# Kernel tuning notes

Measured on AMD Instinct MI355X. Metric: run time of the kernel, lower is better.

The kernel has to match this reference:

```python
import jax, jax.numpy as jnp
import numpy as np

SCALE = 8      # scale_factor from map_to_mat_info
PATCH = 32     # up_delta - low_delta + 1 == right_delta - left_delta + 1 (uniform interior patches)


def setup_inputs() -> dict:
    key = jax.random.key(0)
    mat_h, mat_w = 160, 160
    H = (mat_h - 1) * SCALE + PATCH  # 1304: deltas (0,31,0,31) -> no border clipping
    W = (mat_w - 1) * SCALE + PATCH
    x = jax.random.normal(key, (1, 3, H, W), dtype=jnp.float32)
    rgb_weight = jnp.array([0.299, 0.587, 0.114], dtype=jnp.float32).reshape(1, 3, 1, 1)
    return {"x": x, "rgb_weight": rgb_weight, "mat_h": mat_h, "mat_w": mat_w}


def reference(x, rgb_weight, mat_h, mat_w):
    P = PATCH
    # RGB -> grayscale (convert_gray branch for in_channels == 3)
    gray = jnp.sum(x * rgb_weight, axis=1)[0]  # (H, W)
    # Gather all overlapping PxP patches at stride SCALE -> (mat_h, mat_w, P, P)
    rows = (jnp.arange(mat_h) * SCALE)[:, None] + jnp.arange(P)[None, :]  # (mat_h, P)
    cols = (jnp.arange(mat_w) * SCALE)[:, None] + jnp.arange(P)[None, :]  # (mat_w, P)
    p = gray[rows.reshape(-1)].reshape(mat_h, P, -1)              # (mat_h, P, W)
    p = p[:, :, cols.reshape(-1)].reshape(mat_h, P, mat_w, P)     # (mat_h, P, mat_w, P)
    patches = jnp.transpose(p, (0, 2, 1, 3))                      # (mat_h, mat_w, P, P)
    # torch.rfft(signal_ndim=2, onesided=False) == full 2D FFT; power = re^2 + im^2
    F = jnp.fft.fft2(patches)
    log_power = jnp.log(F.real * F.real + F.imag * F.imag + 1.0)
    # High-frequency region sums (h == w == P, static)
    lo = P // 2 - P // 4 - 1   # 7
    up = P // 2 + P // 4       # 24
    r1 = jnp.sum(log_power[..., lo:up + 1, :], axis=(-2, -1))
    r2 = jnp.sum(log_power[..., up + 1:, lo:up + 1], axis=(-2, -1))
    r3 = jnp.sum(log_power[..., :lo, lo:up + 1], axis=(-2, -1))
    mat = (r1 + r2 + r3)[None, None]  # (1, 1, mat_h, mat_w)
    return mat / jnp.max(mat)
```

## Files before the change

### kernel.cpp

```cpp
#include <hip/hip_runtime.h>
#include <math.h>

#define SCALE 8
#define PSZ 32

__device__ constexpr float C32[16] = {
     1.000000000000000f,  0.980785280403230f,  0.923879532511287f,  0.831469612302545f,
     0.707106781186548f,  0.555570233019602f,  0.382683432365090f,  0.195090322016128f,
     0.000000000000000f, -0.195090322016128f, -0.382683432365090f, -0.555570233019602f,
    -0.707106781186548f, -0.831469612302545f, -0.923879532511287f, -0.980785280403230f };
__device__ constexpr float S32[16] = {
     0.000000000000000f,  0.195090322016128f,  0.382683432365090f,  0.555570233019602f,
     0.707106781186548f,  0.831469612302545f,  0.923879532511287f,  0.980785280403230f,
     1.000000000000000f,  0.980785280403230f,  0.923879532511287f,  0.831469612302545f,
     0.707106781186548f,  0.555570233019602f,  0.382683432365090f,  0.195090322016128f };

__device__ __forceinline__ constexpr int brev4(int i) {
    return ((i & 1) << 3) | ((i & 2) << 1) | ((i & 4) >> 1) | ((i & 8) >> 3);
}

__device__ __forceinline__ void fft16(float re[16], float im[16]) {
#pragma unroll
    for (int i = 0; i < 16; ++i) {
        const int j = brev4(i);
        if (j > i) {
            float t = re[i]; re[i] = re[j]; re[j] = t;
            t = im[i]; im[i] = im[j]; im[j] = t;
        }
    }
#pragma unroll
    for (int s = 1; s <= 4; ++s) {
        const int m = 1 << s;
        const int h = m >> 1;
        const int tstep = 32 >> s;
#pragma unroll
        for (int k = 0; k < 16; k += m) {
#pragma unroll
            for (int j = 0; j < h; ++j) {
                const float wr = C32[j * tstep];
                const float wi = -S32[j * tstep];
                const int a = k + j;
                const int b = k + j + h;
                const float tr = wr * re[b] - wi * im[b];
                const float ti = wr * im[b] + wi * re[b];
                re[b] = re[a] - tr; im[b] = im[a] - ti;
                re[a] = re[a] + tr; im[a] = im[a] + ti;
            }
        }
    }
}

__device__ __forceinline__ unsigned pack_bf2(float hi, float lo) {
    const unsigned uh = __float_as_uint(hi) + 0x8000u;
    const unsigned ul = __float_as_uint(lo) + 0x8000u;
    return (uh & 0xFFFF0000u) | (ul >> 16);
}
__device__ __forceinline__ float bf_hi(unsigned u) { return __uint_as_float(u & 0xFFFF0000u); }
__device__ __forceinline__ float bf_lo(unsigned u) { return __uint_as_float(u << 16); }

__global__ __launch_bounds__(256) void gray_kernel(
        const float* __restrict__ x, const float* __restrict__ w,
        float* __restrict__ g, int n4, long long HW) {
    const int i = blockIdx.x * 256 + threadIdx.x;
    if (i >= n4) return;
    const float w0 = w[0], w1 = w[1], w2 = w[2];
    const float4 a = reinterpret_cast<const float4*>(x)[i];
    const float4 b = reinterpret_cast<const float4*>(x + HW)[i];
    const float4 c = reinterpret_cast<const float4*>(x + 2 * HW)[i];
    float4 o;
    o.x = w0 * a.x + w1 * b.x + w2 * c.x;
    o.y = w0 * a.y + w1 * b.y + w2 * c.y;
    o.z = w0 * a.z + w1 * b.z + w2 * c.z;
    o.w = w0 * a.w + w1 * b.w + w2 * c.w;
    reinterpret_cast<float4*>(g)[i] = o;
}

template <bool GRAY_PRE>
__global__ __launch_bounds__(128) void hfdft_patch_kernel(
        const float* __restrict__ x, const float* __restrict__ w,
        float* __restrict__ out, int H, int W, int mat_h, int mat_w) {
    __shared__ unsigned cb[8 * 528];

    const int tid = threadIdx.x;
    const int wid = tid >> 6;
    const int lane = tid & 63;
    const int P0 = blockIdx.x * 8 + wid * 4;
    const int total = mat_h * mat_w;
    const long long HW = (long long)H * W;
    unsigned* cbw = cb + wid * 4 * 528;

    {
        const int g = lane >> 5, r = lane & 31;
        int pA = P0 + 2 * g;
        if (pA > total - 1) pA = total - 1;
        int pB = pA + 1; if (pB > total - 1) pB = total - 1;
        const int phA = pA / mat_w, pwA = pA % mat_w;
        const int phB = pB / mat_w, pwB = pB % mat_w;
        const bool adj = (phA == phB) && (pwB == pwA + 1);
        const int baseA = (phA * SCALE + r) * W + pwA * SCALE;
        const int baseB = (phB * SCALE + r) * W + pwB * SCALE;
        const float w0 = GRAY_PRE ? 0.0f : w[0];
        const float w1 = GRAY_PRE ? 0.0f : w[1];
        const float w2 = GRAY_PRE ? 0.0f : w[2];

        unsigned* cbA = cbw + (2 * g) * 528;
        unsigned* cbB = cbA + 528;


        {
            float win[40];
            if (GRAY_PRE && adj) {
                const float4* g4 = reinterpret_cast<const float4*>(x + baseA);
#pragma unroll
                for (int q = 0; q < 10; ++q) {
                    const float4 v = g4[q];
                    win[4 * q + 0] = v.x; win[4 * q + 1] = v.y;
                    win[4 * q + 2] = v.z; win[4 * q + 3] = v.w;
                }
            } else if (GRAY_PRE) {
#pragma unroll
                for (int i = 0; i < 32; ++i) win[i] = x[baseA + i];
#pragma unroll
                for (int i = 0; i < 8; ++i) win[32 + i] = 0.0f;
            } else {
#pragma unroll
                for (int i = 0; i < 32; ++i)
                    win[i] = w0 * x[baseA + i] + w1 * x[HW + baseA + i] + w2 * x[2 * HW + baseA + i];
#pragma unroll
                for (int i = 0; i < 8; ++i) win[32 + i] = 0.0f;
            }
            float er[16], ei[16];
            if (GRAY_PRE && adj) {
#pragma unroll
                for (int i = 0; i < 16; ++i) {
                    er[i] = win[i] + win[i + 16];
                    ei[i] = win[i + 8] + win[i + 24];
                }
            } else if (GRAY_PRE) {
#pragma unroll
                for (int i = 0; i < 16; ++i) {
                    er[i] = win[i] + win[i + 16];
                    ei[i] = x[baseB + i] + x[baseB + i + 16];
                }
            } else {
#pragma unroll
                for (int i = 0; i < 16; ++i) {
                    er[i] = win[i] + win[i + 16];
                    const float blo = w0 * x[baseB + i] + w1 * x[HW + baseB + i] + w2 * x[2 * HW + baseB + i];
                    const float bhi = w0 * x[baseB + i + 16] + w1 * x[HW + baseB + i + 16] + w2 * x[2 * HW + baseB + i + 16];
                    ei[i] = blo + bhi;
                }
            }
            fft16(er, ei);
            cbA[r] = pack_bf2(er[0], er[8]);
            cbB[r] = pack_bf2(ei[0], ei[8]);
#pragma unroll
            for (int k2 = 1; k2 <= 7; ++k2) {
                const int e1 = k2, e2 = 16 - k2;
                const float far_ = 0.5f * (er[e1] + er[e2]);
                const float fai_ = 0.5f * (ei[e1] - ei[e2]);
                const float fbr_ = 0.5f * (ei[e1] + ei[e2]);
                const float fbi_ = 0.5f * (er[e2] - er[e1]);
                cbA[(2 * k2) * 33 + r] = pack_bf2(far_, fai_);
                cbB[(2 * k2) * 33 + r] = pack_bf2(fbr_, fbi_);
            }
        }

        asm volatile("" ::: "memory");

        {
            float win[40];
            if (GRAY_PRE && adj) {
                const float4* g4 = reinterpret_cast<const float4*>(x + baseA);
#pragma unroll
                for (int q = 0; q < 10; ++q) {
                    const float4 v = g4[q];
                    win[4 * q + 0] = v.x; win[4 * q + 1] = v.y;
                    win[4 * q + 2] = v.z; win[4 * q + 3] = v.w;
                }
            } else if (GRAY_PRE) {
#pragma unroll
                for (int i = 0; i < 32; ++i) win[i] = x[baseA + i];
#pragma unroll
                for (int i = 0; i < 8; ++i) win[32 + i] = 0.0f;
            } else {
#pragma unroll
                for (int i = 0; i < 32; ++i)
                    win[i] = w0 * x[baseA + i] + w1 * x[HW + baseA + i] + w2 * x[2 * HW + baseA + i];
#pragma unroll
                for (int i = 0; i < 8; ++i) win[32 + i] = 0.0f;
            }
            float orr[16], oi[16];
#pragma unroll
            for (int i = 0; i < 16; ++i) {
                float dre, dim;
                if (GRAY_PRE && adj) {
                    dre = win[i] - win[i + 16];
                    dim = win[i + 8] - win[i + 24];
                } else if (GRAY_PRE) {
                    dre = win[i] - win[i + 16];
                    dim = x[baseB + i] - x[baseB + i + 16];
                } else {
                    dre = win[i] - win[i + 16];
                    const float blo = w0 * x[baseB + i] + w1 * x[HW + baseB + i] + w2 * x[2 * HW + baseB + i];
                    const float bhi = w0 * x[baseB + i + 16] + w1 * x[HW + baseB + i + 16] + w2 * x[2 * HW + baseB + i + 16];
                    dim = blo - bhi;
                }
                orr[i] = dre * C32[i] + dim * S32[i];
                oi[i]  = dim * C32[i] - dre * S32[i];
            }
            fft16(orr, oi);
#pragma unroll
            for (int k2 = 0; k2 <= 7; ++k2) {
                const int o1 = k2, o2 = 15 - k2;
                const float far_ = 0.5f * (orr[o1] + orr[o2]);
                const float fai_ = 0.5f * (oi[o1] - oi[o2]);
                const float fbr_ = 0.5f * (oi[o1] + oi[o2]);
                const float fbi_ = 0.5f * (orr[o2] - orr[o1]);
                cbA[(2 * k2 + 1) * 33 + r] = pack_bf2(far_, fai_);
                cbB[(2 * k2 + 1) * 33 + r] = pack_bf2(fbr_, fbi_);
            }
        }
    }

    asm volatile("s_waitcnt lgkmcnt(0)" ::: "memory");

    {
        const int pl = lane >> 4, slot = lane & 15;
        const int p = P0 + pl;
        const unsigned* cbp = cbw + pl * 528 + slot * 33;
        const float b1f = (slot >= 7) ? 1.0f : 0.0f;
        const float m1f = (slot >= 8) ? 1.0f : 0.0f;

        float s0 = 0.0f, s1 = 0.0f;

        {
            float er[16], ei[16];
#pragma unroll
            for (int i = 0; i < 16; ++i) {
                const unsigned u0 = cbp[i], u1 = cbp[i + 16];
                er[i] = bf_hi(u0) + bf_hi(u1);
                ei[i] = bf_lo(u0) + bf_lo(u1);
            }
            fft16(er, ei);
            if (slot == 0) {
#pragma unroll
                for (int k2 = 0; k2 <= 8; ++k2) {
                    const int kr = 2 * k2;
                    const int a = k2, b = (k2 == 0) ? 0 : 16 - k2;
                    const float g0r = 0.5f * (er[a] + er[b]);
                    const float g0i = 0.5f * (ei[a] - ei[b]);
                    const float g1r = 0.5f * (ei[a] + ei[b]);
                    const float g1i = 0.5f * (er[b] - er[a]);
                    const float w0c = (kr >= 7 ? 1.0f : 0.0f) + ((kr >= 8 && kr <= 15) ? 1.0f : 0.0f);
                    const float w16c = 1.0f + ((kr >= 1 && kr <= 15) ? 1.0f : 0.0f);
                    if (w0c > 0.0f)
                        s0 = fmaf(w0c, __logf(g0r * g0r + g0i * g0i + 1.0f), s0);
                    s1 = fmaf(w16c, __logf(g1r * g1r + g1i * g1i + 1.0f), s1);
                }
            } else {
#pragma unroll
                for (int k2 = 0; k2 < 16; ++k2) {
                    const int kr = 2 * k2;
                    const float lp = __logf(er[k2] * er[k2] + ei[k2] * ei[k2] + 1.0f);
                    const float wgt = (kr >= 8 && kr <= 24) ? 2.0f : (b1f + m1f);
                    if (k2 & 1) s1 = fmaf(wgt, lp, s1);
                    else        s0 = fmaf(wgt, lp, s0);
                }
            }
        }

        asm volatile("" ::: "memory");

        {
            float orr[16], oi[16];
#pragma unroll
            for (int i = 0; i < 16; ++i) {
                const unsigned u0 = cbp[i], u1 = cbp[i + 16];
                const float dre = bf_hi(u0) - bf_hi(u1);
                const float dim = bf_lo(u0) - bf_lo(u1);
                orr[i] = dre * C32[i] + dim * S32[i];
                oi[i]  = dim * C32[i] - dre * S32[i];
            }
            fft16(orr, oi);
            if (slot == 0) {
#pragma unroll
                for (int k2 = 0; k2 <= 7; ++k2) {
                    const int kr = 2 * k2 + 1;
                    const int a = k2, b = 15 - k2;
                    const float g0r = 0.5f * (orr[a] + orr[b]);
                    const float g0i = 0.5f * (oi[a] - oi[b]);
                    const float g1r = 0.5f * (oi[a] + oi[b]);
                    const float g1i = 0.5f * (orr[b] - orr[a]);
                    const float w0c = (kr >= 7 ? 1.0f : 0.0f) + ((kr >= 8 && kr <= 15) ? 1.0f : 0.0f);
                    const float w16c = 2.0f;
                    if (w0c > 0.0f)
                        s0 = fmaf(w0c, __logf(g0r * g0r + g0i * g0i + 1.0f), s0);
                    s1 = fmaf(w16c, __logf(g1r * g1r + g1i * g1i + 1.0f), s1);
                }
            } else {
#pragma unroll
                for (int k2 = 0; k2 < 16; ++k2) {
                    const int kr = 2 * k2 + 1;
                    const float lp = __logf(orr[k2] * orr[k2] + oi[k2] * oi[k2] + 1.0f);
                    float wgt;
                    if (kr == 7)                   wgt = 1.0f + m1f;
                    else if (kr == 25)             wgt = b1f + 1.0f;
                    else if (kr >= 9 && kr <= 23)  wgt = 2.0f;
                    else                           wgt = b1f + m1f;
                    if (k2 & 1) s1 = fmaf(wgt, lp, s1);
                    else        s0 = fmaf(wgt, lp, s0);
                }
            }
        }

        float s = s0 + s1;
#pragma unroll
        for (int off = 8; off >= 1; off >>= 1) s += __shfl_xor(s, off, 16);
        if (slot == 0 && p < total) out[p] = s;
    }
}

__global__ __launch_bounds__(1024) void max_kernel(
        const float* __restrict__ sums, int n, float* __restrict__ partial) {
    __shared__ float sm[16];
    float m = 0.0f;
    for (int i = blockIdx.x * 1024 + threadIdx.x; i < n; i += gridDim.x * 1024)
        m = fmaxf(m, sums[i]);
#pragma unroll
    for (int off = 32; off >= 1; off >>= 1) m = fmaxf(m, __shfl_xor(m, off, 64));
    if ((threadIdx.x & 63) == 0) sm[threadIdx.x >> 6] = m;
    __syncthreads();
    if (threadIdx.x == 0) {
#pragma unroll
        for (int i = 1; i < 16; ++i) m = fmaxf(m, sm[i]);
        partial[blockIdx.x] = m;
    }
}

__global__ __launch_bounds__(256) void norm_kernel(
        float* __restrict__ out, int n, const float* __restrict__ partial) {
    const int i = blockIdx.x * 256 + threadIdx.x;
    float m = partial[0];
#pragma unroll
    for (int b = 1; b < 8; ++b) m = fmaxf(m, partial[b]);
    if (i < n) out[i] = out[i] / m;
}

extern "C" void kernel_launch(void* const* d_in, const int* in_sizes, int n_in,
                              void* d_out, int out_size, void* d_ws, size_t ws_size,
                              hipStream_t stream) {
    const float* x = (const float*)d_in[0];
    const float* w = (const float*)d_in[1];
    float* out = (float*)d_out;

    const int HWi = in_sizes[0] / 3;
    const int H = (int)(sqrt((double)HWi) + 0.5);
    const int W = H;
    const long long HW = (long long)H * W;
    const int mat = (int)(sqrt((double)out_size) + 0.5);
    const int total = mat * mat;
    const int blocksA = (total + 7) / 8;

    float* partial = (float*)d_ws;
    float* gray = (float*)((char*)d_ws + 256);
    const size_t need = 256 + (size_t)HW * 4;

    if (ws_size >= need && (W & 3) == 0) {
        const int n4 = (int)(HW / 4);
        hipLaunchKernelGGL(gray_kernel, dim3((n4 + 255) / 256), dim3(256), 0, stream,
                           x, w, gray, n4, HW);
        hipLaunchKernelGGL((hfdft_patch_kernel<true>), dim3(blocksA), dim3(128), 0, stream,
                           gray, w, out, H, W, mat, mat);
    } else {
        hipLaunchKernelGGL((hfdft_patch_kernel<false>), dim3(blocksA), dim3(128), 0, stream,
                           x, w, out, H, W, mat, mat);
    }
    hipLaunchKernelGGL(max_kernel, dim3(8), dim3(1024), 0, stream, out, total, partial);
    hipLaunchKernelGGL(norm_kernel, dim3((total + 255) / 256), dim3(256), 0, stream,
                       out, total, partial);
}
```

Measured before the change: 46.02 us.

## Split even/odd FFT halves across two wavefronts per patch group

```diff
diff --git a/kernel.cpp b/kernel.cpp
--- a/kernel.cpp
+++ b/kernel.cpp
@@ -79,19 +79,19 @@
 __global__ __launch_bounds__(128) void hfdft_patch_kernel(
         const float* __restrict__ x, const float* __restrict__ w,
         float* __restrict__ out, int H, int W, int mat_h, int mat_w) {
-    __shared__ unsigned cb[8 * 528];
+    __shared__ unsigned cb[4 * 528];
+    __shared__ float red[8];
 
     const int tid = threadIdx.x;
-    const int wid = tid >> 6;
+    const int h = tid >> 6;
     const int lane = tid & 63;
-    const int P0 = blockIdx.x * 8 + wid * 4;
     const int total = mat_h * mat_w;
     const long long HW = (long long)H * W;
-    unsigned* cbw = cb + wid * 4 * 528;
+    const int Pbase = blockIdx.x * 4;
 
     {
         const int g = lane >> 5, r = lane & 31;
-        int pA = P0 + 2 * g;
+        int pA = Pbase + 2 * g;
         if (pA > total - 1) pA = total - 1;
         int pB = pA + 1; if (pB > total - 1) pB = total - 1;
         const int phA = pA / mat_w, pwA = pA % mat_w;
@@ -99,159 +99,119 @@
         const bool adj = (phA == phB) && (pwB == pwA + 1);
         const int baseA = (phA * SCALE + r) * W + pwA * SCALE;
         const int baseB = (phB * SCALE + r) * W + pwB * SCALE;
-        const float w0 = GRAY_PRE ? 0.0f : w[0];
-        const float w1 = GRAY_PRE ? 0.0f : w[1];
-        const float w2 = GRAY_PRE ? 0.0f : w[2];
-
-        unsigned* cbA = cbw + (2 * g) * 528;
+
+        float ar[32], br[32];
+        if (GRAY_PRE && adj) {
+            float win[40];
+            const float4* g4 = reinterpret_cast<const float4*>(x + baseA);
+#pragma unroll
+            for (int q = 0; q < 10; ++q) {
+                const float4 v = g4[q];
+                win[4 * q + 0] = v.x; win[4 * q + 1] = v.y;
+                win[4 * q + 2] = v.z; win[4 * q + 3] = v.w;
+            }
+#pragma unroll
+            for (int i = 0; i < 32; ++i) { ar[i] = win[i]; br[i] = win[i + 8]; }
+        } else if (GRAY_PRE) {
+#pragma unroll
+            for (int i = 0; i < 32; ++i) { ar[i] = x[baseA + i]; br[i] = x[baseB + i]; }
+        } else {
+            const float w0 = w[0], w1 = w[1], w2 = w[2];
+#pragma unroll
+            for (int i = 0; i < 32; ++i) {
+                ar[i] = w0 * x[baseA + i] + w1 * x[HW + baseA + i] + w2 * x[2 * HW + baseA + i];
+                br[i] = w0 * x[baseB + i] + w1 * x[HW + baseB + i] + w2 * x[2 * HW + baseB + i];
+            }
+        }
+
+        float fr[16], fi[16];
+        if (h == 0) {
+#pragma unroll
+            for (int i = 0; i < 16; ++i) {
+                fr[i] = ar[i] + ar[i + 16];
+                fi[i] = br[i] + br[i + 16];
+            }
+        } else {
+#pragma unroll
+            for (int i = 0; i < 16; ++i) {
+                const float dre = ar[i] - ar[i + 16];
+                const float dim = br[i] - br[i + 16];
+                fr[i] = dre * C32[i] + dim * S32[i];
+                fi[i] = dim * C32[i] - dre * S32[i];
+            }
+        }
+
+        fft16(fr, fi);
+
+        unsigned* cbA = cb + (2 * g) * 528;
         unsigned* cbB = cbA + 528;
-
-
-        {
-            float win[40];
-            if (GRAY_PRE && adj) {
-                const float4* g4 = reinterpret_cast<const float4*>(x + baseA);
-#pragma unroll
-                for (int q = 0; q < 10; ++q) {
-                    const float4 v = g4[q];
-                    win[4 * q + 0] = v.x; win[4 * q + 1] = v.y;
-                    win[4 * q + 2] = v.z; win[4 * q + 3] = v.w;
-                }
-            } else if (GRAY_PRE) {
-#pragma unroll
-                for (int i = 0; i < 32; ++i) win[i] = x[baseA + i];
-#pragma unroll
-                for (int i = 0; i < 8; ++i) win[32 + i] = 0.0f;
-            } else {
-#pragma unroll
-                for (int i = 0; i < 32; ++i)
-                    win[i] = w0 * x[baseA + i] + w1 * x[HW + baseA + i] + w2 * x[2 * HW + baseA + i];
-#pragma unroll
-                for (int i = 0; i < 8; ++i) win[32 + i] = 0.0f;
-            }
-            float er[16], ei[16];
-            if (GRAY_PRE && adj) {
-#pragma unroll
-                for (int i = 0; i < 16; ++i) {
-                    er[i] = win[i] + win[i + 16];
-                    ei[i] = win[i + 8] + win[i + 24];
-                }
-            } else if (GRAY_PRE) {
-#pragma unroll
-                for (int i = 0; i < 16; ++i) {
-                    er[i] = win[i] + win[i + 16];
-                    ei[i] = x[baseB + i] + x[baseB + i + 16];
-                }
-            } else {
-#pragma unroll
-                for (int i = 0; i < 16; ++i) {
-                    er[i] = win[i] + win[i + 16];
-                    const float blo = w0 * x[baseB + i] + w1 * x[HW + baseB + i] + w2 * x[2 * HW + baseB + i];
-                    const float bhi = w0 * x[baseB + i + 16] + w1 * x[HW + baseB + i + 16] + w2 * x[2 * HW + baseB + i + 16];
-                    ei[i] = blo + bhi;
-                }
-            }
-            fft16(er, ei);
-            cbA[r] = pack_bf2(er[0], er[8]);
-            cbB[r] = pack_bf2(ei[0], ei[8]);
+        if (h == 0) {
+            cbA[r] = pack_bf2(fr[0], fr[8]);
+            cbB[r] = pack_bf2(fi[0], fi[8]);
 #pragma unroll
             for (int k2 = 1; k2 <= 7; ++k2) {
-                const int e1 = k2, e2 = 16 - k2;
-                const float far_ = 0.5f * (er[e1] + er[e2]);
-                const float fai_ = 0.5f * (ei[e1] - ei[e2]);
-                const float fbr_ = 0.5f * (ei[e1] + ei[e2]);
-                const float fbi_ = 0.5f * (er[e2] - er[e1]);
+                const int e2 = 16 - k2;
+                const float far_ = 0.5f * (fr[k2] + fr[e2]);
+                const float fai_ = 0.5f * (fi[k2] - fi[e2]);
+                const float fbr_ = 0.5f * (fi[k2] + fi[e2]);
+                const float fbi_ = 0.5f * (fr[e2] - fr[k2]);
                 cbA[(2 * k2) * 33 + r] = pack_bf2(far_, fai_);
                 cbB[(2 * k2) * 33 + r] = pack_bf2(fbr_, fbi_);
             }
-        }
-
-        asm volatile("" ::: "memory");
-
-        {
-            float win[40];
-            if (GRAY_PRE && adj) {
-                const float4* g4 = reinterpret_cast<const float4*>(x + baseA);
-#pragma unroll
-                for (int q = 0; q < 10; ++q) {
-                    const float4 v = g4[q];
-                    win[4 * q + 0] = v.x; win[4 * q + 1] = v.y;
-                    win[4 * q + 2] = v.z; win[4 * q + 3] = v.w;
-                }
-            } else if (GRAY_PRE) {
-#pragma unroll
-                for (int i = 0; i < 32; ++i) win[i] = x[baseA + i];
-#pragma unroll
-                for (int i = 0; i < 8; ++i) win[32 + i] = 0.0f;
-            } else {
-#pragma unroll
-                for (int i = 0; i < 32; ++i)
-                    win[i] = w0 * x[baseA + i] + w1 * x[HW + baseA + i] + w2 * x[2 * HW + baseA + i];
-#pragma unroll
-                for (int i = 0; i < 8; ++i) win[32 + i] = 0.0f;
-            }
-            float orr[16], oi[16];
-#pragma unroll
-            for (int i = 0; i < 16; ++i) {
-                float dre, dim;
-                if (GRAY_PRE && adj) {
-                    dre = win[i] - win[i + 16];
-                    dim = win[i + 8] - win[i + 24];
-                } else if (GRAY_PRE) {
-                    dre = win[i] - win[i + 16];
-                    dim = x[baseB + i] - x[baseB + i + 16];
-                } else {
-                    dre = win[i] - win[i + 16];
-                    const float blo = w0 * x[baseB + i] + w1 * x[HW + baseB + i] + w2 * x[2 * HW + baseB + i];
-                    const float bhi = w0 * x[baseB + i + 16] + w1 * x[HW + baseB + i + 16] + w2 * x[2 * HW + baseB + i + 16];
-                    dim = blo - bhi;
-                }
-                orr[i] = dre * C32[i] + dim * S32[i];
-                oi[i]  = dim * C32[i] - dre * S32[i];
-            }
-            fft16(orr, oi);
+        } else {
 #pragma unroll
             for (int k2 = 0; k2 <= 7; ++k2) {
-                const int o1 = k2, o2 = 15 - k2;
-                const float far_ = 0.5f * (orr[o1] + orr[o2]);
-                const float fai_ = 0.5f * (oi[o1] - oi[o2]);
-                const float fbr_ = 0.5f * (oi[o1] + oi[o2]);
-                const float fbi_ = 0.5f * (orr[o2] - orr[o1]);
+                const int o2 = 15 - k2;
+                const float far_ = 0.5f * (fr[k2] + fr[o2]);
+                const float fai_ = 0.5f * (fi[k2] - fi[o2]);
+                const float fbr_ = 0.5f * (fi[k2] + fi[o2]);
+                const float fbi_ = 0.5f * (fr[o2] - fr[k2]);
                 cbA[(2 * k2 + 1) * 33 + r] = pack_bf2(far_, fai_);
                 cbB[(2 * k2 + 1) * 33 + r] = pack_bf2(fbr_, fbi_);
             }
         }
     }
 
-    asm volatile("s_waitcnt lgkmcnt(0)" ::: "memory");
+    __syncthreads();
 
     {
         const int pl = lane >> 4, slot = lane & 15;
-        const int p = P0 + pl;
-        const unsigned* cbp = cbw + pl * 528 + slot * 33;
-        const float b1f = (slot >= 7) ? 1.0f : 0.0f;
-        const float m1f = (slot >= 8) ? 1.0f : 0.0f;
-
-        float s0 = 0.0f, s1 = 0.0f;
-
-        {
-            float er[16], ei[16];
+        int p = Pbase + pl;
+        if (p > total - 1) p = total - 1;
+        const unsigned* cbp = cb + pl * 528 + slot * 33;
+
+        float fr[16], fi[16];
+        if (h == 0) {
 #pragma unroll
             for (int i = 0; i < 16; ++i) {
                 const unsigned u0 = cbp[i], u1 = cbp[i + 16];
-                er[i] = bf_hi(u0) + bf_hi(u1);
-                ei[i] = bf_lo(u0) + bf_lo(u1);
-            }
-            fft16(er, ei);
-            if (slot == 0) {
+                fr[i] = bf_hi(u0) + bf_hi(u1);
+                fi[i] = bf_lo(u0) + bf_lo(u1);
+            }
+        } else {
+#pragma unroll
+            for (int i = 0; i < 16; ++i) {
+                const unsigned u0 = cbp[i], u1 = cbp[i + 16];
+                const float dre = bf_hi(u0) - bf_hi(u1);
+                const float dim = bf_lo(u0) - bf_lo(u1);
+                fr[i] = dre * C32[i] + dim * S32[i];
+                fi[i] = dim * C32[i] - dre * S32[i];
+            }
+        }
+
+        fft16(fr, fi);
+
+        float s0 = 0.0f, s1 = 0.0f;
+        if (slot == 0) {
+            if (h == 0) {
 #pragma unroll
                 for (int k2 = 0; k2 <= 8; ++k2) {
                     const int kr = 2 * k2;
-                    const int a = k2, b = (k2 == 0) ? 0 : 16 - k2;
-                    const float g0r = 0.5f * (er[a] + er[b]);
-                    const float g0i = 0.5f * (ei[a] - ei[b]);
-                    const float g1r = 0.5f * (ei[a] + ei[b]);
-                    const float g1i = 0.5f * (er[b] - er[a]);
+                    const int b = (k2 == 0) ? 0 : 16 - k2;
+                    const float g0r = 0.5f * (fr[k2] + fr[b]);
+                    const float g0i = 0.5f * (fi[k2] - fi[b]);
+                    const float g1r = 0.5f * (fi[k2] + fi[b]);
+                    const float g1i = 0.5f * (fr[b] - fr[k2]);
                     const float w0c = (kr >= 7 ? 1.0f : 0.0f) + ((kr >= 8 && kr <= 15) ? 1.0f : 0.0f);
                     const float w16c = 1.0f + ((kr >= 1 && kr <= 15) ? 1.0f : 0.0f);
                     if (w0c > 0.0f)
@@ -260,49 +220,37 @@
                 }
             } else {
 #pragma unroll
-                for (int k2 = 0; k2 < 16; ++k2) {
-                    const int kr = 2 * k2;
-                    const float lp = __logf(er[k2] * er[k2] + ei[k2] * ei[k2] + 1.0f);
-                    const float wgt = (kr >= 8 && kr <= 24) ? 2.0f : (b1f + m1f);
-                    if (k2 & 1) s1 = fmaf(wgt, lp, s1);
-                    else        s0 = fmaf(wgt, lp, s0);
-                }
-            }
-        }
-
-        asm volatile("" ::: "memory");
-
-        {
-            float orr[16], oi[16];
-#pragma unroll
-            for (int i = 0; i < 16; ++i) {
-                const unsigned u0 = cbp[i], u1 = cbp[i + 16];
-                const float dre = bf_hi(u0) - bf_hi(u1);
-                const float dim = bf_lo(u0) - bf_lo(u1);
-                orr[i] = dre * C32[i] + dim * S32[i];
-                oi[i]  = dim * C32[i] - dre * S32[i];
-            }
-            fft16(orr, oi);
-            if (slot == 0) {
-#pragma unroll
                 for (int k2 = 0; k2 <= 7; ++k2) {
                     const int kr = 2 * k2 + 1;
-                    const int a = k2, b = 15 - k2;
-                    const float g0r = 0.5f * (orr[a] + orr[b]);
-                    const float g0i = 0.5f * (oi[a] - oi[b]);
-                    const float g1r = 0.5f * (oi[a] + oi[b]);
-                    const float g1i = 0.5f * (orr[b] - orr[a]);
+                    const int b = 15 - k2;
+                    const float g0r = 0.5f * (fr[k2] + fr[b]);
+                    const float g0i = 0.5f * (fi[k2] - fi[b]);
+                    const float g1r = 0.5f * (fi[k2] + fi[b]);
+                    const float g1i = 0.5f * (fr[b] - fr[k2]);
                     const float w0c = (kr >= 7 ? 1.0f : 0.0f) + ((kr >= 8 && kr <= 15) ? 1.0f : 0.0f);
                     const float w16c = 2.0f;
                     if (w0c > 0.0f)
                         s0 = fmaf(w0c, __logf(g0r * g0r + g0i * g0i + 1.0f), s0);
                     s1 = fmaf(w16c, __logf(g1r * g1r + g1i * g1i + 1.0f), s1);
                 }
+            }
+        } else {
+            const float b1f = (slot >= 7) ? 1.0f : 0.0f;
+            const float m1f = (slot >= 8) ? 1.0f : 0.0f;
+            if (h == 0) {
+#pragma unroll
+                for (int k2 = 0; k2 < 16; ++k2) {
+                    const int kr = 2 * k2;
+                    const float lp = __logf(fr[k2] * fr[k2] + fi[k2] * fi[k2] + 1.0f);
+                    const float wgt = (kr >= 8 && kr <= 24) ? 2.0f : (b1f + m1f);
+                    if (k2 & 1) s1 = fmaf(wgt, lp, s1);
+                    else        s0 = fmaf(wgt, lp, s0);
+                }
             } else {
 #pragma unroll
                 for (int k2 = 0; k2 < 16; ++k2) {
                     const int kr = 2 * k2 + 1;
-                    const float lp = __logf(orr[k2] * orr[k2] + oi[k2] * oi[k2] + 1.0f);
+                    const float lp = __logf(fr[k2] * fr[k2] + fi[k2] * fi[k2] + 1.0f);
                     float wgt;
                     if (kr == 7)                   wgt = 1.0f + m1f;
                     else if (kr == 25)             wgt = b1f + 1.0f;
@@ -317,7 +265,14 @@
         float s = s0 + s1;
 #pragma unroll
         for (int off = 8; off >= 1; off >>= 1) s += __shfl_xor(s, off, 16);
-        if (slot == 0 && p < total) out[p] = s;
+        if (slot == 0) red[pl * 2 + h] = s;
+    }
+
+    __syncthreads();
+
+    if (tid < 4) {
+        const int p = Pbase + tid;
+        if (p < total) out[p] = red[tid * 2] + red[tid * 2 + 1];
     }
 }
 
@@ -360,7 +315,7 @@
     const long long HW = (long long)H * W;
     const int mat = (int)(sqrt((double)out_size) + 0.5);
     const int total = mat * mat;
-    const int blocksA = (total + 7) / 8;
+    const int blocksA = (total + 3) / 4;
 
     float* partial = (float*)d_ws;
     float* gray = (float*)((char*)d_ws + 256);
```

New measurement: 47.90 us. 4.1% more time.
